# Optimization experiments

Measured on AMD Instinct MI355X. Metric: run time of the kernel, lower is better.

Reference implementation:

```python
import jax, jax.numpy as jnp
import numpy as np

B = 4096
N_COL = 100      # all-numerical columns
N_COND = 64      # d*m = 4*16
D = 4
TOTAL = N_COL * N_COND   # 6400
N_RODT = TOTAL // D      # 1600
N_EST = 160              # max(2,int(sqrt(100))) * N_COND // D
N_FOREST = 100
N_HIDDEN = 128
N_CLASS = 10
EPS = 1e-5


def group_norm(x, w, b, groups):
    # x: [B, C] (spatial dim of 1 dropped); normalize within each channel group
    Bn, C = x.shape
    xg = x.reshape(Bn, groups, C // groups)
    mu = xg.mean(-1, keepdims=True)
    var = ((xg - mu) ** 2).mean(-1, keepdims=True)
    xn = ((xg - mu) * jax.lax.rsqrt(var + EPS)).reshape(Bn, C)
    return xn * w + b


def layer_norm(x, w, b):
    mu = x.mean(-1, keepdims=True)
    var = ((x - mu) ** 2).mean(-1, keepdims=True)
    return (x - mu) * jax.lax.rsqrt(var + EPS) * w + b


def setup_inputs() -> dict:
    key = jax.random.key(0)
    ks = jax.random.split(key, 16)
    s = 0.3  # weight scale
    x = jax.random.normal(ks[0], (B, N_COL), jnp.float32)
    w1 = jax.random.normal(ks[1], (N_COL, N_COND), jnp.float32) * s
    b1 = jax.random.normal(ks[2], (N_COL, N_COND), jnp.float32) * s
    perm = jax.random.permutation(ks[3], TOTAL)
    gn1_w = jnp.ones((TOTAL,), jnp.float32)
    gn1_b = jnp.zeros((TOTAL,), jnp.float32)
    conv2_w = jax.random.normal(ks[4], (N_RODT, D, D), jnp.float32) * s
    conv2_b = jax.random.normal(ks[5], (TOTAL,), jnp.float32) * s
    gn2_w = jnp.ones((TOTAL,), jnp.float32)
    gn2_b = jnp.zeros((TOTAL,), jnp.float32)
    conv3_w = jax.random.normal(ks[6], (N_RODT, D, 1), jnp.float32) * s
    conv3_b = jax.random.normal(ks[7], (N_RODT,), jnp.float32) * s
    # sample-without-replacement per forest (eval-mode fixed indices)
    swr = jax.vmap(lambda k: jax.random.permutation(k, N_RODT)[:N_EST])(
        jax.random.split(ks[8], N_FOREST))
    E = jax.random.normal(ks[9], (N_RODT, N_HIDDEN), jnp.float32)
    ln1_w = jnp.ones((N_HIDDEN,), jnp.float32)
    ln1_b = jnp.zeros((N_HIDDEN,), jnp.float32)
    fc1_w = jax.random.normal(ks[10], (N_HIDDEN, N_HIDDEN), jnp.float32) * (1.0 / np.sqrt(N_HIDDEN))
    fc1_b = jnp.zeros((N_HIDDEN,), jnp.float32)
    ln2_w = jnp.ones((N_HIDDEN,), jnp.float32)
    ln2_b = jnp.zeros((N_HIDDEN,), jnp.float32)
    fc2_w = jax.random.normal(ks[11], (N_HIDDEN, N_CLASS), jnp.float32) * (1.0 / np.sqrt(N_HIDDEN))
    fc2_b = jnp.zeros((N_CLASS,), jnp.float32)
    return dict(x=x, w1=w1, b1=b1, perm=perm, gn1_w=gn1_w, gn1_b=gn1_b,
                conv2_w=conv2_w, conv2_b=conv2_b, gn2_w=gn2_w, gn2_b=gn2_b,
                conv3_w=conv3_w, conv3_b=conv3_b, swr=swr, E=E,
                ln1_w=ln1_w, ln1_b=ln1_b, fc1_w=fc1_w, fc1_b=fc1_b,
                ln2_w=ln2_w, ln2_b=ln2_b, fc2_w=fc2_w, fc2_b=fc2_b)


def reference(x, w1, b1, perm, gn1_w, gn1_b, conv2_w, conv2_b, gn2_w, gn2_b,
              conv3_w, conv3_b, swr, E, ln1_w, ln1_b, fc1_w, fc1_b,
              ln2_w, ln2_b, fc2_w, fc2_b):
    b = x.shape[0]
    # --- ConditionGeneration (numerical path): per-column 1->n_cond group conv + sigmoid
    M = jax.nn.sigmoid(x[:, :, None] * w1[None] + b1[None])        # [B, n_col, n_cond]
    M = M.transpose(0, 2, 1)                                        # [B, n_cond, n_col]
    # --- rODTConstruction: flatten + fixed permutation
    O = M.reshape(b, -1)[:, perm]                                   # [B, total]
    # --- phi_2: GN -> grouped 4->4 conv -> ReLU -> GN -> grouped 4->1 conv
    h = group_norm(O, gn1_w, gn1_b, N_RODT)
    h = jnp.einsum('bgi,gio->bgo', h.reshape(b, N_RODT, D), conv2_w).reshape(b, TOTAL) + conv2_b
    h = jax.nn.relu(h)
    h = group_norm(h, gn2_w, gn2_b, N_RODT)
    w = jnp.einsum('bgi,gio->bgo', h.reshape(b, N_RODT, D), conv3_w)[..., 0] + conv3_b  # [B, n_rodt] (n_head=1)
    # --- rODT forest: gather estimators, softmax over estimators, weighted sum of rODT embeddings
    ws = jax.nn.softmax(w[:, swr], axis=2)                          # [B, n_forest, n_est]
    Ep = E[swr]                                                     # [n_forest, n_est, n_hidden]
    F = jnp.einsum('bfe,fed->bfd', ws, Ep)                          # [B, n_forest, n_hidden]
    # --- bagging MLP (dropout=0)
    h2 = layer_norm(F, ln1_w, ln1_b)
    h2 = jax.nn.relu(h2 @ fc1_w + fc1_b)
    h2 = layer_norm(h2, ln2_w, ln2_b)
    y_hat = h2 @ fc2_w + fc2_b                                      # [B, n_forest, n_class]
    return y_hat.mean(1)                                            # [B, n_class]
```

## Files before the change

### kernel.cpp

```cpp
#include <hip/hip_runtime.h>
#include <hip/hip_bf16.h>
#include <stdint.h>

#define NB 4096
#define NCOL 100
#define NCOND 64
#define NTOTAL 6400
#define NRODT 1600
#define NEST 160
#define NFOR 100
#define NHID 128
#define NCLS 10
#define GEPS 1e-5f

typedef __attribute__((ext_vector_type(8))) short short8;
typedef __attribute__((ext_vector_type(4))) float floatx4;

__device__ __forceinline__ unsigned f2bfu(float x) {
  union { float f; unsigned u; } v; v.f = x;
  return (v.u + 0x8000u) >> 16;
}
__device__ __forceinline__ float bf2f(unsigned short u) {
  union { unsigned u; float f; } v; v.u = ((unsigned)u) << 16;
  return v.f;
}

__global__ __launch_bounds__(256) void k01_prep(
    const float* __restrict__ x, const float* __restrict__ w1,
    const float* __restrict__ b1, const int* __restrict__ perm,
    const float* __restrict__ gn1w, const float* __restrict__ gn1b,
    const float* __restrict__ c2w, const float* __restrict__ c2b,
    const float* __restrict__ gn2w, const float* __restrict__ gn2b,
    const float* __restrict__ c3w, const float* __restrict__ c3b,
    const float* __restrict__ E, const int* __restrict__ swr,
    const float* __restrict__ fc1w, const float* __restrict__ fc2w,
    unsigned short* __restrict__ wT,
    unsigned short* __restrict__ Bf, unsigned short* __restrict__ W1f,
    unsigned short* __restrict__ W2f, float* __restrict__ out)
{
  __shared__ float xl[64 * NCOL];
  __shared__ int ridx[NEST];
  const int tid = threadIdx.x;
  const int blk = blockIdx.x;

  if (blk < 1600) {
    const int b0 = (blk & 63) * 64;
    const int g  = (blk >> 6) * 64 + (tid >> 2);
    const int i4 = tid & 3;
    for (int i = tid; i < 64 * NCOL; i += 256)
      xl[i] = x[(size_t)b0 * NCOL + i];
    __syncthreads();

    const int4 p4 = *(const int4*)(perm + 4 * g);
    const int pv[4] = {p4.x, p4.y, p4.z, p4.w};
    float w1v[4], b1v[4];
    int pc[4];
#pragma unroll
    for (int i = 0; i < 4; i++) {
      unsigned p = (unsigned)pv[i];
      unsigned j = p / 100u;
      unsigned cc = p - j * 100u;
      pc[i] = (int)cc;
      w1v[i] = w1[cc * NCOND + j];
      b1v[i] = b1[cc * NCOND + j];
    }
    const float4 g1w = *(const float4*)(gn1w + 4 * g);
    const float4 g1b = *(const float4*)(gn1b + 4 * g);
    const float4 cw0 = *(const float4*)(c2w + 16 * g);
    const float4 cw1 = *(const float4*)(c2w + 16 * g + 4);
    const float4 cw2 = *(const float4*)(c2w + 16 * g + 8);
    const float4 cw3 = *(const float4*)(c2w + 16 * g + 12);
    const float4 cbv = *(const float4*)(c2b + 4 * g);
    const float4 g2w = *(const float4*)(gn2w + 4 * g);
    const float4 g2b = *(const float4*)(gn2b + 4 * g);
    const float4 c3v = *(const float4*)(c3w + 4 * g);
    const float c3bv = c3b[g];

    for (int k = 0; k < 4; k++) {
      float v4[4];
#pragma unroll
      for (int j = 0; j < 4; j++) {
        const int bb = k * 16 + i4 * 4 + j;
        float O[4];
#pragma unroll
        for (int i = 0; i < 4; i++) {
          float a = xl[bb * NCOL + pc[i]] * w1v[i] + b1v[i];
          O[i] = 1.0f / (1.0f + __expf(-a));
        }
        float mu = 0.25f * (O[0] + O[1] + O[2] + O[3]);
        float d[4], var = 0.f;
#pragma unroll
        for (int i = 0; i < 4; i++) { d[i] = O[i] - mu; var += d[i] * d[i]; }
        float rs = rsqrtf(0.25f * var + GEPS);
        float xn0 = d[0] * rs * g1w.x + g1b.x;
        float xn1 = d[1] * rs * g1w.y + g1b.y;
        float xn2 = d[2] * rs * g1w.z + g1b.z;
        float xn3 = d[3] * rs * g1w.w + g1b.w;
        float h[4];
        h[0] = xn0*cw0.x + xn1*cw1.x + xn2*cw2.x + xn3*cw3.x + cbv.x;
        h[1] = xn0*cw0.y + xn1*cw1.y + xn2*cw2.y + xn3*cw3.y + cbv.y;
        h[2] = xn0*cw0.z + xn1*cw1.z + xn2*cw2.z + xn3*cw3.z + cbv.z;
        h[3] = xn0*cw0.w + xn1*cw1.w + xn2*cw2.w + xn3*cw3.w + cbv.w;
#pragma unroll
        for (int i = 0; i < 4; i++) h[i] = fmaxf(h[i], 0.f);
        float mu2 = 0.25f * (h[0] + h[1] + h[2] + h[3]);
        float e[4], var2 = 0.f;
#pragma unroll
        for (int i = 0; i < 4; i++) { e[i] = h[i] - mu2; var2 += e[i] * e[i]; }
        float rs2 = rsqrtf(0.25f * var2 + GEPS);
        float hn0 = e[0] * rs2 * g2w.x + g2b.x;
        float hn1 = e[1] * rs2 * g2w.y + g2b.y;
        float hn2 = e[2] * rs2 * g2w.z + g2b.z;
        float hn3 = e[3] * rs2 * g2w.w + g2b.w;
        v4[j] = hn0*c3v.x + hn1*c3v.y + hn2*c3v.z + hn3*c3v.w + c3bv;
      }
      uint2 pk;
      pk.x = f2bfu(v4[0]) | (f2bfu(v4[1]) << 16);
      pk.y = f2bfu(v4[2]) | (f2bfu(v4[3]) << 16);
      *(uint2*)(wT + (size_t)g * NB + b0 + k * 16 + i4 * 4) = pk;
    }
  } else if (blk < 1600 + NFOR) {
    const int fblk = blk - 1600;
    if (tid < NEST) ridx[tid] = swr[fblk * NEST + tid];
    __syncthreads();
    for (int m = tid; m < 2560; m += 256) {
      int lane = m & 63, rest = m >> 6;
      int kc = rest % 5, n = rest / 5;
      int q = lane >> 4, c = lane & 15;
      int e0 = kc * 32 + q * 8;
      int h = n * 16 + c;
      union { unsigned short v[8]; uint4 u; } t;
#pragma unroll
      for (int j = 0; j < 8; j++)
        t.v[j] = (unsigned short)f2bfu(E[(size_t)ridx[e0 + j] * NHID + h]);
      *(uint4*)(Bf + (size_t)fblk * 20480 + (size_t)m * 8) = t.u;
    }
  } else if (blk == 1600 + NFOR) {
    for (int m = tid; m < 2048; m += 256) {
      int lane = m & 63, rest = m >> 6;
      int kc = rest & 3, n = rest >> 2;
      int q = lane >> 4, c = lane & 15;
      int k0 = kc * 32 + q * 8;
      int o = n * 16 + c;
      union { unsigned short v[8]; uint4 u; } t;
#pragma unroll
      for (int j = 0; j < 8; j++)
        t.v[j] = (unsigned short)f2bfu(fc1w[(size_t)(k0 + j) * NHID + o]);
      *(uint4*)(W1f + (size_t)m * 8) = t.u;
    }
  } else if (blk == 1601 + NFOR) {
    for (int m = tid; m < 256; m += 256) {
      int lane = m & 63, kc = m >> 6;
      int q = lane >> 4, c = lane & 15;
      int k0 = kc * 32 + q * 8;
      union { unsigned short v[8]; uint4 u; } t;
#pragma unroll
      for (int j = 0; j < 8; j++)
        t.v[j] = (unsigned short)f2bfu(c < NCLS ? fc2w[(size_t)(k0 + j) * NCLS + c] : 0.f);
      *(uint4*)(W2f + (size_t)m * 8) = t.u;
    }
  } else {
    const int z = blk - (1602 + NFOR);
    float4 zz = make_float4(0.f, 0.f, 0.f, 0.f);
    for (int i = z * 256 + tid; i < NB * NCLS / 4; i += 3 * 256)
      ((float4*)out)[i] = zz;
  }
}

__global__ __launch_bounds__(256, 6) void k3_mfma(
    const unsigned short* __restrict__ wT,
    const int* __restrict__ swr,
    const unsigned short* __restrict__ Bf,
    const unsigned short* __restrict__ W1f,
    const unsigned short* __restrict__ W2f,
    const float* __restrict__ ln1w, const float* __restrict__ ln1b,
    const float* __restrict__ fc1b,
    const float* __restrict__ ln2w, const float* __restrict__ ln2b,
    const float* __restrict__ fc2b,
    float* __restrict__ out)
{
  __shared__ unsigned short lsA[64 * 168];
  __shared__ int ridx[NEST];

  const int tid = threadIdx.x;
  const int f  = blockIdx.x;
  const int b0 = blockIdx.y * 64;
  const int lane = tid & 63, wv = tid >> 6;
  const int c = lane & 15, q = lane >> 4;

  if (tid < NEST) ridx[tid] = swr[f * NEST + tid];
  __syncthreads();

  const int r = tid >> 2, ch = tid & 3;
  const unsigned short* wcol = wT + b0 + r;
  const int* rp = ridx + ch * 40;
  float g[40];
#pragma unroll
  for (int j = 0; j < 40; j++)
    g[j] = bf2f(wcol[(size_t)rp[j] * NB]);

  float mx = -1e30f;
#pragma unroll
  for (int j = 0; j < 40; j++) mx = fmaxf(mx, g[j]);
  mx = fmaxf(mx, __shfl_xor(mx, 1));
  mx = fmaxf(mx, __shfl_xor(mx, 2));
  float s = 0.f;
#pragma unroll
  for (int j = 0; j < 40; j++) { g[j] = __expf(g[j] - mx); s += g[j]; }
  s += __shfl_xor(s, 1);
  s += __shfl_xor(s, 2);
  const float inv = 1.0f / s;

  unsigned* dst = (unsigned*)(lsA + r * 168) + ch * 20;
#pragma unroll
  for (int k = 0; k < 20; k++) {
    unsigned u0 = f2bfu(g[2 * k] * inv);
    unsigned u1 = f2bfu(g[2 * k + 1] * inv);
    dst[k] = u0 | (u1 << 16);
  }

  const unsigned short* pa = lsA + (wv * 16 + c) * 168 + q * 8;
  floatx4 acc[8];
#pragma unroll
  for (int n = 0; n < 8; n++) acc[n] = (floatx4){0.f, 0.f, 0.f, 0.f};

  const unsigned short* bbase = Bf + (size_t)f * 20480 + lane * 8;
#pragma unroll
  for (int kc = 0; kc < 5; kc++) {
    short8 a = *(const short8*)(pa + kc * 32);
#pragma unroll
    for (int n = 0; n < 8; n++) {
      short8 b = *(const short8*)(bbase + n * 2560 + kc * 512);
      acc[n] = __builtin_amdgcn_mfma_f32_16x16x32_bf16(a, b, acc[n], 0, 0, 0);
    }
  }

  {
    float lw[8], lb[8];
#pragma unroll
    for (int n = 0; n < 8; n++) { lw[n] = ln1w[n * 16 + c]; lb[n] = ln1b[n * 16 + c]; }
#pragma unroll
    for (int rr = 0; rr < 4; rr++) {
      float s1 = 0.f, s2 = 0.f;
#pragma unroll
      for (int n = 0; n < 8; n++) { float v = acc[n][rr]; s1 += v; s2 += v * v; }
#pragma unroll
      for (int off = 1; off < 16; off <<= 1) {
        s1 += __shfl_xor(s1, off); s2 += __shfl_xor(s2, off);
      }
      float mu = s1 * (1.f / 128.f);
      float var = fmaxf(s2 * (1.f / 128.f) - mu * mu, 0.f);
      float rs = rsqrtf(var + GEPS);
#pragma unroll
      for (int n = 0; n < 8; n++)
        acc[n][rr] = (acc[n][rr] - mu) * rs * lw[n] + lb[n];
    }
  }

#pragma unroll
  for (int rr = 0; rr < 4; rr++)
#pragma unroll
    for (int n = 0; n < 8; n++)
      lsA[(wv * 16 + q * 4 + rr) * 168 + n * 16 + c] =
          (unsigned short)f2bfu(acc[n][rr]);

  {
    short8 a0 = *(const short8*)(pa);
    short8 a1 = *(const short8*)(pa + 32);
    short8 a2 = *(const short8*)(pa + 64);
    short8 a3 = *(const short8*)(pa + 96);
#pragma unroll
    for (int n = 0; n < 8; n++) acc[n] = (floatx4){0.f, 0.f, 0.f, 0.f};
    const unsigned short* w1p = W1f + lane * 8;
#pragma unroll
    for (int n = 0; n < 8; n++) {
      const unsigned short* wp = w1p + n * 2048;
      acc[n] = __builtin_amdgcn_mfma_f32_16x16x32_bf16(a0, *(const short8*)(wp),        acc[n], 0, 0, 0);
      acc[n] = __builtin_amdgcn_mfma_f32_16x16x32_bf16(a1, *(const short8*)(wp + 512),  acc[n], 0, 0, 0);
      acc[n] = __builtin_amdgcn_mfma_f32_16x16x32_bf16(a2, *(const short8*)(wp + 1024), acc[n], 0, 0, 0);
      acc[n] = __builtin_amdgcn_mfma_f32_16x16x32_bf16(a3, *(const short8*)(wp + 1536), acc[n], 0, 0, 0);
    }
  }

  {
    float fb[8], lw[8], lb[8];
#pragma unroll
    for (int n = 0; n < 8; n++) {
      fb[n] = fc1b[n * 16 + c];
      lw[n] = ln2w[n * 16 + c]; lb[n] = ln2b[n * 16 + c];
    }
#pragma unroll
    for (int rr = 0; rr < 4; rr++) {
#pragma unroll
      for (int n = 0; n < 8; n++) acc[n][rr] = fmaxf(acc[n][rr] + fb[n], 0.f);
      float s1 = 0.f, s2 = 0.f;
#pragma unroll
      for (int n = 0; n < 8; n++) { float v = acc[n][rr]; s1 += v; s2 += v * v; }
#pragma unroll
      for (int off = 1; off < 16; off <<= 1) {
        s1 += __shfl_xor(s1, off); s2 += __shfl_xor(s2, off);
      }
      float mu = s1 * (1.f / 128.f);
      float var = fmaxf(s2 * (1.f / 128.f) - mu * mu, 0.f);
      float rs = rsqrtf(var + GEPS);
#pragma unroll
      for (int n = 0; n < 8; n++)
        acc[n][rr] = (acc[n][rr] - mu) * rs * lw[n] + lb[n];
    }
  }

#pragma unroll
  for (int rr = 0; rr < 4; rr++)
#pragma unroll
    for (int n = 0; n < 8; n++)
      lsA[(wv * 16 + q * 4 + rr) * 168 + n * 16 + c] =
          (unsigned short)f2bfu(acc[n][rr]);

  floatx4 o4 = (floatx4){0.f, 0.f, 0.f, 0.f};
#pragma unroll
  for (int kc = 0; kc < 4; kc++) {
    short8 a = *(const short8*)(pa + kc * 32);
    short8 b = *(const short8*)(W2f + kc * 512 + lane * 8);
    o4 = __builtin_amdgcn_mfma_f32_16x16x32_bf16(a, b, o4, 0, 0, 0);
  }
  if (c < NCLS) {
    float bias = fc2b[c];
#pragma unroll
    for (int rr = 0; rr < 4; rr++)
      atomicAdd(out + (size_t)(b0 + wv * 16 + q * 4 + rr) * NCLS + c,
                (o4[rr] + bias) * 0.01f);
  }
}

extern "C" void kernel_launch(void* const* d_in, const int* in_sizes, int n_in,
                              void* d_out, int out_size, void* d_ws, size_t ws_size,
                              hipStream_t stream)
{
  (void)in_sizes; (void)n_in; (void)ws_size; (void)out_size;
  const float* x    = (const float*)d_in[0];
  const float* w1   = (const float*)d_in[1];
  const float* b1   = (const float*)d_in[2];
  const int*   perm = (const int*)d_in[3];
  const float* gn1w = (const float*)d_in[4];
  const float* gn1b = (const float*)d_in[5];
  const float* c2w  = (const float*)d_in[6];
  const float* c2b  = (const float*)d_in[7];
  const float* gn2w = (const float*)d_in[8];
  const float* gn2b = (const float*)d_in[9];
  const float* c3w  = (const float*)d_in[10];
  const float* c3b  = (const float*)d_in[11];
  const int*   swr  = (const int*)d_in[12];
  const float* E    = (const float*)d_in[13];
  const float* ln1w = (const float*)d_in[14];
  const float* ln1b = (const float*)d_in[15];
  const float* fc1w = (const float*)d_in[16];
  const float* fc1b = (const float*)d_in[17];
  const float* ln2w = (const float*)d_in[18];
  const float* ln2b = (const float*)d_in[19];
  const float* fc2w = (const float*)d_in[20];
  const float* fc2b = (const float*)d_in[21];
  float* out = (float*)d_out;

  const size_t W_BYTES = (size_t)NB * NRODT * 2;
  unsigned short* wTbuf = (unsigned short*)d_ws;
  unsigned short* Bfb   = (unsigned short*)((char*)d_ws + W_BYTES);
  unsigned short* W1fb  = (unsigned short*)((char*)d_ws + W_BYTES + 4096000);
  unsigned short* W2fb  = (unsigned short*)((char*)d_ws + W_BYTES + 4096000 + 32768);

  k01_prep<<<1600 + NFOR + 2 + 3, 256, 0, stream>>>(
      x, w1, b1, perm, gn1w, gn1b, c2w, c2b, gn2w, gn2b, c3w, c3b,
      E, swr, fc1w, fc2w, wTbuf, Bfb, W1fb, W2fb, out);
  dim3 g3(NFOR, NB / 64);
  k3_mfma<<<g3, 256, 0, stream>>>(wTbuf, swr, Bfb, W1fb, W2fb,
                                  ln1w, ln1b, fc1b, ln2w, ln2b, fc2b, out);
}
```

Baseline: 254.8 us.

## Coalesce softmax gathers, defer normalization past MFMA, and swap grid order

The softmax gather is rewritten so each wave takes 40 estimators and each lane takes one batch row. The 64 lanes of a wave then read contiguous bf16 values from the transposed weight buffer, and each lane writes 16-byte packed stores into LDS. The max subtraction is dropped. Unnormalized exponentials feed the MFMA, and per-row sums from shared memory are applied to the accumulators afterwards. The grid is swapped so that consecutive blocks share a forest, which improves L2 reuse of its B fragments, and a barrier is added before the MFMA reads LDS. Skipping the max subtraction risks overflow if the logits grow large.

```diff
diff --git a/kernel.cpp b/kernel.cpp
--- a/kernel.cpp
+++ b/kernel.cpp
@@ -181,43 +181,42 @@
 {
   __shared__ unsigned short lsA[64 * 168];
   __shared__ int ridx[NEST];
+  __shared__ float sP[4][64];
 
   const int tid = threadIdx.x;
-  const int f  = blockIdx.x;
-  const int b0 = blockIdx.y * 64;
+  const int b0 = blockIdx.x * 64;
+  const int f  = blockIdx.y;
   const int lane = tid & 63, wv = tid >> 6;
   const int c = lane & 15, q = lane >> 4;
 
   if (tid < NEST) ridx[tid] = swr[f * NEST + tid];
   __syncthreads();
 
-  const int r = tid >> 2, ch = tid & 3;
-  const unsigned short* wcol = wT + b0 + r;
-  const int* rp = ridx + ch * 40;
-  float g[40];
-#pragma unroll
-  for (int j = 0; j < 40; j++)
-    g[j] = bf2f(wcol[(size_t)rp[j] * NB]);
-
-  float mx = -1e30f;
-#pragma unroll
-  for (int j = 0; j < 40; j++) mx = fmaxf(mx, g[j]);
-  mx = fmaxf(mx, __shfl_xor(mx, 1));
-  mx = fmaxf(mx, __shfl_xor(mx, 2));
-  float s = 0.f;
-#pragma unroll
-  for (int j = 0; j < 40; j++) { g[j] = __expf(g[j] - mx); s += g[j]; }
-  s += __shfl_xor(s, 1);
-  s += __shfl_xor(s, 2);
-  const float inv = 1.0f / s;
-
-  unsigned* dst = (unsigned*)(lsA + r * 168) + ch * 20;
-#pragma unroll
-  for (int k = 0; k < 20; k++) {
-    unsigned u0 = f2bfu(g[2 * k] * inv);
-    unsigned u1 = f2bfu(g[2 * k + 1] * inv);
-    dst[k] = u0 | (u1 << 16);
-  }
+  {
+    const unsigned short* wbase = wT + b0 + lane;
+    float ssum = 0.f;
+#pragma unroll
+    for (int k = 0; k < 5; k++) {
+      unsigned pk0, pk1, pk2, pk3;
+      unsigned us[8];
+#pragma unroll
+      for (int jj = 0; jj < 8; jj++) {
+        const int e = wv * 40 + k * 8 + jj;
+        float v = bf2f(wbase[(size_t)ridx[e] * NB]);
+        float ex = __expf(v);
+        ssum += ex;
+        us[jj] = f2bfu(ex);
+      }
+      pk0 = us[0] | (us[1] << 16);
+      pk1 = us[2] | (us[3] << 16);
+      pk2 = us[4] | (us[5] << 16);
+      pk3 = us[6] | (us[7] << 16);
+      uint4 pk = {pk0, pk1, pk2, pk3};
+      *(uint4*)(lsA + lane * 168 + wv * 40 + k * 8) = pk;
+    }
+    sP[wv][lane] = ssum;
+  }
+  __syncthreads();
 
   const unsigned short* pa = lsA + (wv * 16 + c) * 168 + q * 8;
   floatx4 acc[8];
@@ -232,6 +231,17 @@
     for (int n = 0; n < 8; n++) {
       short8 b = *(const short8*)(bbase + n * 2560 + kc * 512);
       acc[n] = __builtin_amdgcn_mfma_f32_16x16x32_bf16(a, b, acc[n], 0, 0, 0);
+    }
+  }
+
+  {
+#pragma unroll
+    for (int rr = 0; rr < 4; rr++) {
+      const int row = wv * 16 + q * 4 + rr;
+      float st = sP[0][row] + sP[1][row] + sP[2][row] + sP[3][row];
+      float invs = 1.0f / st;
+#pragma unroll
+      for (int n = 0; n < 8; n++) acc[n][rr] *= invs;
     }
   }
 
@@ -370,7 +380,7 @@
   k01_prep<<<1600 + NFOR + 2 + 3, 256, 0, stream>>>(
       x, w1, b1, perm, gn1w, gn1b, c2w, c2b, gn2w, gn2b, c3w, c3b,
       E, swr, fc1w, fc2w, wTbuf, Bfb, W1fb, W2fb, out);
-  dim3 g3(NFOR, NB / 64);
+  dim3 g3(NB / 64, NFOR);
   k3_mfma<<<g3, 256, 0, stream>>>(wTbuf, swr, Bfb, W1fb, W2fb,
                                   ln1w, ln1b, fc1b, ln2w, ln2b, fc2b, out);
 }
```

Result: faster. 236.5 us (-7.2%).
